# Kernel tuning notes

Hardware: AMD Instinct MI355X
Metric: run time of the kernel (lower is better)

Reference implementation:

```python
import jax, jax.numpy as jnp
import numpy as np

N = 50000      # nodes
E = 800000     # directed edges (avg degree 16)
F_IN = 128     # dataset.num_features
H = 256        # hidden_channels
C = 40         # dataset.num_classes


def _glorot(k, shape):
    lim = float(np.sqrt(6.0 / (shape[0] + shape[1])))
    return jax.random.uniform(k, shape, jnp.float32, -lim, lim)


def setup_inputs() -> dict:
    key = jax.random.key(0)
    ks = jax.random.split(key, 8)
    x = jax.random.normal(ks[0], (N, F_IN), jnp.float32)
    edge_index = jax.random.randint(ks[1], (2, E), 0, N, dtype=jnp.int32)
    W1 = _glorot(ks[2], (F_IN, H));      b1 = jnp.zeros((H,), jnp.float32)
    W2 = _glorot(ks[3], (H, H // 2));    b2 = jnp.zeros((H // 2,), jnp.float32)
    W3 = _glorot(ks[4], (H // 2, H // 4)); b3 = jnp.zeros((H // 4,), jnp.float32)
    W4 = _glorot(ks[5], (H // 4, C));    b4 = jnp.zeros((C,), jnp.float32)
    return {"x": x, "edge_index": edge_index,
            "W1": W1, "b1": b1, "W2": W2, "b2": b2,
            "W3": W3, "b3": b3, "W4": W4, "b4": b4}


def reference(x, edge_index, W1, b1, W2, b2, W3, b3, W4, b4):
    # GCNConv with default add_self_loops=True and symmetric normalization.
    loops = jnp.arange(N, dtype=edge_index.dtype)
    src = jnp.concatenate([edge_index[0], loops])   # message sources
    dst = jnp.concatenate([edge_index[1], loops])   # aggregation targets
    # degree computed on target index (PyG default), incl. self-loops
    deg = jax.ops.segment_sum(jnp.ones_like(dst, jnp.float32), dst, num_segments=N)
    dinv = jnp.where(deg > 0, jax.lax.rsqrt(deg), 0.0)
    norm = dinv[src] * dinv[dst]                    # [E+N]

    def conv(h, W, b):
        h = h @ W                                   # transform first (PyG order)
        msg = h[src] * norm[:, None]                # gather + scale
        return jax.ops.segment_sum(msg, dst, num_segments=N) + b

    h = jax.nn.relu(conv(x, W1, b1))   # dropout = identity in eval mode
    h = jax.nn.relu(conv(h, W2, b2))
    h = jax.nn.relu(conv(h, W3, b3))
    return conv(h, W4, b4)
```

## Files before the change

kernel.cpp:

```cpp
#include <hip/hip_runtime.h>
#include <stdint.h>

#define NNODES 50000
#define NEDGES 800000
#define NB ((NNODES + 255) / 256)
#define EPB 4096
#define SCAT_NBLK ((NEDGES + EPB - 1) / EPB)

typedef __attribute__((ext_vector_type(8))) short bf16x8;
typedef __attribute__((ext_vector_type(4))) float f32x4;

__device__ inline unsigned short f2bf(float f) {
    unsigned u = __float_as_uint(f);
    return (unsigned short)((u + 0x7fffu + ((u >> 16) & 1u)) >> 16);
}
__device__ inline float bf2f(unsigned short h) {
    return __uint_as_float(((unsigned)h) << 16);
}


__global__ void zero_kernel(int* __restrict__ p, int n) {
    int i = blockIdx.x * blockDim.x + threadIdx.x;
    if (i < n) p[i] = 0;
}

__global__ __launch_bounds__(256) void bucket_count_kernel(const int* __restrict__ dst,
                                                           int* __restrict__ bhist) {
    __shared__ int h[NB];
    for (int b = threadIdx.x; b < NB; b += 256) h[b] = 0;
    __syncthreads();
    const int base = blockIdx.x * EPB;
#pragma unroll
    for (int i = 0; i < EPB / 256; ++i) {
        const int e = base + threadIdx.x + i * 256;
        if (e < NEDGES) atomicAdd(&h[dst[e] >> 8], 1);
    }
    __syncthreads();
    for (int b = threadIdx.x; b < NB; b += 256)
        if (h[b]) atomicAdd(&bhist[b], h[b]);
}

__global__ __launch_bounds__(256) void bucket_scan_kernel(const int* __restrict__ bhist,
                                                          int* __restrict__ bofs,
                                                          int* __restrict__ gcur,
                                                          int* __restrict__ rp_last) {
    __shared__ int s[256];
    const int t = threadIdx.x;
    s[t] = (t < NB) ? bhist[t] : 0;
    __syncthreads();
    for (int off = 1; off < 256; off <<= 1) {
        int v = (t >= off) ? s[t - off] : 0;
        __syncthreads();
        s[t] += v;
        __syncthreads();
    }
    if (t < NB) {
        const int excl = (t > 0) ? s[t - 1] : 0;
        bofs[t] = excl;
        gcur[t] = excl;
    }
    if (t == 255) { bofs[NB] = s[255]; rp_last[0] = s[255]; }
}

__global__ __launch_bounds__(256) void bucket_scatter_kernel(const int* __restrict__ src,
                                                             const int* __restrict__ dst,
                                                             int* __restrict__ gcur,
                                                             unsigned* __restrict__ gpk) {
    __shared__ int h[256];
    __shared__ int s[256];
    __shared__ int gof[256];
    __shared__ unsigned pr[EPB];
    __shared__ int ga[EPB];

    const int t = threadIdx.x;
    const int base = blockIdx.x * EPB;
    const int nval = min(EPB, NEDGES - base);

    h[t] = 0;
    __syncthreads();
#pragma unroll
    for (int i = 0; i < EPB / 256; ++i) {
        const int e = base + t + i * 256;
        if (e < NEDGES) atomicAdd(&h[dst[e] >> 8], 1);
    }
    __syncthreads();
    s[t] = h[t];
    __syncthreads();
    for (int off = 1; off < 256; off <<= 1) {
        int v = (t >= off) ? s[t - off] : 0;
        __syncthreads();
        s[t] += v;
        __syncthreads();
    }
    {
        const int c = h[t];
        if (t < NB && c > 0) gof[t] = atomicAdd(&gcur[t], c);
        const int lofs = s[t] - c;
        h[t] = lofs;
        s[t] = lofs;
    }
    __syncthreads();
#pragma unroll
    for (int i = 0; i < EPB / 256; ++i) {
        const int e = base + t + i * 256;
        if (e < NEDGES) {
            const int d = dst[e];
            const int b = d >> 8;
            const int slot = atomicAdd(&h[b], 1);
            pr[slot] = ((unsigned)(d & 255) << 16) | (unsigned)src[e];
            ga[slot] = gof[b] + (slot - s[b]);
        }
    }
    __syncthreads();
#pragma unroll
    for (int i = 0; i < EPB / 256; ++i) {
        const int slot = t + i * 256;
        if (slot < nval) gpk[ga[slot]] = pr[slot];
    }
}

__global__ __launch_bounds__(256) void csr_fill_kernel(const unsigned* __restrict__ gpk,
                                                       const int* __restrict__ bofs,
                                                       int* __restrict__ rp,
                                                       float* __restrict__ dinv,
                                                       unsigned short* __restrict__ col) {
    __shared__ int c[256];
    __shared__ int s[256];
    __shared__ int cur[256];
    const int t = threadIdx.x;
    const int b = blockIdx.x;
    const int beg = bofs[b], end = bofs[b + 1];
    c[t] = 0;
    __syncthreads();
    for (int e = beg + t; e < end; e += 256) atomicAdd(&c[gpk[e] >> 16], 1);
    __syncthreads();
    s[t] = c[t];
    __syncthreads();
    for (int off = 1; off < 256; off <<= 1) {
        int v = (t >= off) ? s[t - off] : 0;
        __syncthreads();
        s[t] += v;
        __syncthreads();
    }
    const int excl = s[t] - c[t];
    cur[t] = excl;
    const int node = b * 256 + t;
    if (node < NNODES) {
        rp[node] = beg + excl;
        dinv[node] = rsqrtf((float)(c[t] + 1));
    }
    __syncthreads();
    for (int e = beg + t; e < end; e += 256) {
        const unsigned p = gpk[e];
        const int r = atomicAdd(&cur[p >> 16], 1);
        col[beg + r] = (unsigned short)(p & 0xffffu);
    }
}


__global__ __launch_bounds__(256) void cvt_kernel(const float* __restrict__ in,
                                                  const float* __restrict__ dinv,
                                                  unsigned short* __restrict__ out, int n4) {
    int i = blockIdx.x * 256 + threadIdx.x;
    if (i >= n4) return;
    const float dv = dinv[i >> 5];
    float4 v = *(const float4*)(in + (size_t)i * 4);
    ushort4 h;
    h.x = f2bf(dv * v.x); h.y = f2bf(dv * v.y); h.z = f2bf(dv * v.z); h.w = f2bf(dv * v.w);
    *(ushort4*)(out + (size_t)i * 4) = h;
}


template <bool RELU, bool HAS_BIAS>
__global__ __launch_bounds__(256) void agg128_kernel(const float* __restrict__ in32,
                                                     const unsigned short* __restrict__ inbf,
                                                     float* __restrict__ out,
                                                     const int* __restrict__ rp,
                                                     const unsigned short* __restrict__ col,
                                                     const float* __restrict__ dinv,
                                                     const float* __restrict__ bias) {
    const int wave = threadIdx.x >> 6;
    const int lane = threadIdx.x & 63;
    const int d = blockIdx.x * 4 + wave;
    if (d >= NNODES) return;
    const int quarter = lane >> 4;
    const int fl = lane & 15;
    const float dv = dinv[d];

    float acc[8] = {0.f, 0.f, 0.f, 0.f, 0.f, 0.f, 0.f, 0.f};
    if (quarter == 0) {
        float4 s0 = *(const float4*)(in32 + (size_t)d * 128 + fl * 8);
        float4 s1 = *(const float4*)(in32 + (size_t)d * 128 + fl * 8 + 4);
        acc[0] = dv * s0.x; acc[1] = dv * s0.y; acc[2] = dv * s0.z; acc[3] = dv * s0.w;
        acc[4] = dv * s1.x; acc[5] = dv * s1.y; acc[6] = dv * s1.z; acc[7] = dv * s1.w;
    }

    int j = rp[d] + quarter;
    const int end = rp[d + 1];
    for (; j + 12 < end; j += 16) {
        const int c0 = col[j], c1 = col[j + 4], c2 = col[j + 8], c3 = col[j + 12];
        bf16x8 a0 = *(const bf16x8*)(inbf + (size_t)c0 * 128 + fl * 8);
        bf16x8 a1 = *(const bf16x8*)(inbf + (size_t)c1 * 128 + fl * 8);
        bf16x8 a2 = *(const bf16x8*)(inbf + (size_t)c2 * 128 + fl * 8);
        bf16x8 a3 = *(const bf16x8*)(inbf + (size_t)c3 * 128 + fl * 8);
#pragma unroll
        for (int k = 0; k < 8; ++k)
            acc[k] += (bf2f((unsigned short)a0[k]) + bf2f((unsigned short)a1[k])) +
                      (bf2f((unsigned short)a2[k]) + bf2f((unsigned short)a3[k]));
    }
    for (; j + 4 < end; j += 8) {
        const int c0 = col[j], c1 = col[j + 4];
        bf16x8 a0 = *(const bf16x8*)(inbf + (size_t)c0 * 128 + fl * 8);
        bf16x8 a1 = *(const bf16x8*)(inbf + (size_t)c1 * 128 + fl * 8);
#pragma unroll
        for (int k = 0; k < 8; ++k)
            acc[k] += bf2f((unsigned short)a0[k]) + bf2f((unsigned short)a1[k]);
    }
    if (j < end) {
        const int c0 = col[j];
        bf16x8 a0 = *(const bf16x8*)(inbf + (size_t)c0 * 128 + fl * 8);
#pragma unroll
        for (int k = 0; k < 8; ++k) acc[k] += bf2f((unsigned short)a0[k]);
    }

#pragma unroll
    for (int v = 0; v < 8; ++v) {
        acc[v] += __shfl_down(acc[v], 32);
        acc[v] += __shfl_down(acc[v], 16);
    }

    if (quarter == 0) {
        float r[8];
#pragma unroll
        for (int v = 0; v < 8; ++v) {
            float t = dv * acc[v];
            if constexpr (HAS_BIAS) t += bias[fl * 8 + v];
            if constexpr (RELU) t = fmaxf(t, 0.0f);
            r[v] = t;
        }
        *(float4*)(out + (size_t)d * 128 + fl * 8)     = make_float4(r[0], r[1], r[2], r[3]);
        *(float4*)(out + (size_t)d * 128 + fl * 8 + 4) = make_float4(r[4], r[5], r[6], r[7]);
    }
}

template <bool RELU, bool HAS_BIAS, bool WRITE_BF>
__global__ __launch_bounds__(256) void agg64_kernel(const float* __restrict__ in32,
                                                    const unsigned short* __restrict__ inbf,
                                                    float* __restrict__ out,
                                                    unsigned short* __restrict__ outbf,
                                                    const int* __restrict__ rp,
                                                    const unsigned short* __restrict__ col,
                                                    const float* __restrict__ dinv,
                                                    const float* __restrict__ bias) {
    const int wave = threadIdx.x >> 6;
    const int lane = threadIdx.x & 63;
    const int d = blockIdx.x * 4 + wave;
    if (d >= NNODES) return;
    const int eighth = lane >> 3;
    const int fl = lane & 7;
    const float dv = dinv[d];

    float acc[8] = {0.f, 0.f, 0.f, 0.f, 0.f, 0.f, 0.f, 0.f};
    if (eighth == 0) {
        float4 s0 = *(const float4*)(in32 + (size_t)d * 64 + fl * 8);
        float4 s1 = *(const float4*)(in32 + (size_t)d * 64 + fl * 8 + 4);
        acc[0] = dv * s0.x; acc[1] = dv * s0.y; acc[2] = dv * s0.z; acc[3] = dv * s0.w;
        acc[4] = dv * s1.x; acc[5] = dv * s1.y; acc[6] = dv * s1.z; acc[7] = dv * s1.w;
    }

    int j = rp[d] + eighth;
    const int end = rp[d + 1];
    for (; j + 8 < end; j += 16) {
        const int c0 = col[j], c1 = col[j + 8];
        bf16x8 a0 = *(const bf16x8*)(inbf + (size_t)c0 * 64 + fl * 8);
        bf16x8 a1 = *(const bf16x8*)(inbf + (size_t)c1 * 64 + fl * 8);
#pragma unroll
        for (int k = 0; k < 8; ++k)
            acc[k] += bf2f((unsigned short)a0[k]) + bf2f((unsigned short)a1[k]);
    }
    if (j < end) {
        const int c0 = col[j];
        bf16x8 a0 = *(const bf16x8*)(inbf + (size_t)c0 * 64 + fl * 8);
#pragma unroll
        for (int k = 0; k < 8; ++k) acc[k] += bf2f((unsigned short)a0[k]);
    }

#pragma unroll
    for (int v = 0; v < 8; ++v) {
        acc[v] += __shfl_down(acc[v], 32);
        acc[v] += __shfl_down(acc[v], 16);
        acc[v] += __shfl_down(acc[v], 8);
    }

    if (eighth == 0) {
        float r[8];
#pragma unroll
        for (int v = 0; v < 8; ++v) {
            float t = dv * acc[v];
            if constexpr (HAS_BIAS) t += bias[fl * 8 + v];
            if constexpr (RELU) t = fmaxf(t, 0.0f);
            r[v] = t;
        }
        *(float4*)(out + (size_t)d * 64 + fl * 8)     = make_float4(r[0], r[1], r[2], r[3]);
        *(float4*)(out + (size_t)d * 64 + fl * 8 + 4) = make_float4(r[4], r[5], r[6], r[7]);
        if constexpr (WRITE_BF) {
            ushort4 h0, h1;
            h0.x = f2bf(dv * r[0]); h0.y = f2bf(dv * r[1]);
            h0.z = f2bf(dv * r[2]); h0.w = f2bf(dv * r[3]);
            h1.x = f2bf(dv * r[4]); h1.y = f2bf(dv * r[5]);
            h1.z = f2bf(dv * r[6]); h1.w = f2bf(dv * r[7]);
            *(ushort4*)(outbf + (size_t)d * 64 + fl * 8)     = h0;
            *(ushort4*)(outbf + (size_t)d * 64 + fl * 8 + 4) = h1;
        }
    }
}


template <int K, int M>
__global__ __launch_bounds__(256) void repack_kernel(const float* __restrict__ W,
                                                     unsigned short* __restrict__ hi,
                                                     unsigned short* __restrict__ lo) {
    int i = blockIdx.x * 256 + threadIdx.x;
    if (i >= K * M) return;
    const int k = i / M, n = i % M;
    constexpr int KS = K / 32;
    const int cb = n >> 7;
    const int ct = (n >> 4) & 7;
    const int ln = ((k >> 3) & 3) * 16 + (n & 15);
    const int j  = k & 7;
    const int ks = k >> 5;
    const size_t o = ((((size_t)cb * KS + ks) * 8 + ct) * 64 + ln) * 8 + j;
    const float f = W[i];
    const unsigned short h = f2bf(f);
    hi[o] = h;
    lo[o] = f2bf(f - bf2f(h));
}


template <int K, int M, int BM, bool BIAS_RELU, bool WRITE_BF>
__global__ __launch_bounds__(256) void mfma_gemm_kernel(const float* __restrict__ A,
                                                        const unsigned short* __restrict__ Whi,
                                                        const unsigned short* __restrict__ Wlo,
                                                        const float* __restrict__ bias,
                                                        float* __restrict__ C,
                                                        unsigned short* __restrict__ Cbf,
                                                        const float* __restrict__ dinv) {
    constexpr int KS = K / 32;
    constexpr int ASZ = BM * 64;
    constexpr int CI = (BM == 128) ? 4 : 2;
    __shared__ char lds[2 * ASZ + 16384];
    char* Ahi = lds;
    char* Alo = lds + ASZ;
    char* Bhi = lds + 2 * ASZ;
    char* Blo = lds + 2 * ASZ + 8192;

    const int t = threadIdx.x;
    const int lane = t & 63;
    const int w = t >> 6;
    const int wr = (BM == 128) ? (w >> 1) : 0;
    const int wc = (BM == 128) ? (w & 1) : w;
    const int r0 = blockIdx.x * BM;
    const int n0 = blockIdx.y * 128;

    const unsigned short* bhg = Whi + (size_t)blockIdx.y * KS * 4096;
    const unsigned short* blg = Wlo + (size_t)blockIdx.y * KS * 4096;

    f32x4 acc[4][CI];
#pragma unroll
    for (int i = 0; i < 4; ++i)
#pragma unroll
        for (int j = 0; j < CI; ++j) acc[i][j] = (f32x4){0.f, 0.f, 0.f, 0.f};

    for (int ks = 0; ks < KS; ++ks) {
        const int k0 = ks * 32;

        {
            const char* gh = (const char*)(bhg + (size_t)ks * 4096);
            const char* gl = (const char*)(blg + (size_t)ks * 4096);
#pragma unroll
            for (int c = 0; c < 2; ++c) {
                const int ct = w * 2 + c;
                __builtin_amdgcn_global_load_lds(
                    (const __attribute__((address_space(1))) void*)(gh + ct * 1024 + lane * 16),
                    (__attribute__((address_space(3))) void*)(Bhi + ct * 1024), 16, 0, 0);
                __builtin_amdgcn_global_load_lds(
                    (const __attribute__((address_space(1))) void*)(gl + ct * 1024 + lane * 16),
                    (__attribute__((address_space(3))) void*)(Blo + ct * 1024), 16, 0, 0);
            }
        }

        float4 av[BM / 32];
#pragma unroll
        for (int i = 0; i < BM / 32; ++i) {
            const int q = t + i * 256;
            const int row = q >> 3;
            const int kq = (q & 7) * 4;
            const int gr = r0 + row;
            float4 v = make_float4(0.f, 0.f, 0.f, 0.f);
            if (gr < NNODES) v = *(const float4*)(A + (size_t)gr * K + k0 + kq);
            av[i] = v;
        }
#pragma unroll
        for (int i = 0; i < BM / 32; ++i) {
            const int q = t + i * 256;
            const int row = q >> 3;
            const int kq = (q & 7) * 4;
            const int rt = row >> 4, m = row & 15, quad = kq >> 3, j0 = kq & 7;
            const int off = rt * 1024 + (quad * 16 + m) * 16 + j0 * 2;
            const float4 v = av[i];
            ushort4 h, l;
            h.x = f2bf(v.x); l.x = f2bf(v.x - bf2f(h.x));
            h.y = f2bf(v.y); l.y = f2bf(v.y - bf2f(h.y));
            h.z = f2bf(v.z); l.z = f2bf(v.z - bf2f(h.z));
            h.w = f2bf(v.w); l.w = f2bf(v.w - bf2f(h.w));
            *(ushort4*)(Ahi + off) = h;
            *(ushort4*)(Alo + off) = l;
        }
        __syncthreads();

        bf16x8 ah[4], al[4], bh[CI], bl[CI];
#pragma unroll
        for (int i = 0; i < 4; ++i) {
            ah[i] = *(const bf16x8*)(Ahi + (wr * 4 + i) * 1024 + lane * 16);
            al[i] = *(const bf16x8*)(Alo + (wr * 4 + i) * 1024 + lane * 16);
        }
#pragma unroll
        for (int j = 0; j < CI; ++j) {
            bh[j] = *(const bf16x8*)(Bhi + (wc * CI + j) * 1024 + lane * 16);
            bl[j] = *(const bf16x8*)(Blo + (wc * CI + j) * 1024 + lane * 16);
        }
#pragma unroll
        for (int i = 0; i < 4; ++i)
#pragma unroll
            for (int j = 0; j < CI; ++j) {
                acc[i][j] = __builtin_amdgcn_mfma_f32_16x16x32_bf16(ah[i], bh[j], acc[i][j], 0, 0, 0);
                acc[i][j] = __builtin_amdgcn_mfma_f32_16x16x32_bf16(ah[i], bl[j], acc[i][j], 0, 0, 0);
                acc[i][j] = __builtin_amdgcn_mfma_f32_16x16x32_bf16(al[i], bh[j], acc[i][j], 0, 0, 0);
            }
        __syncthreads();
    }

    const int quad = lane >> 4;
    const int cl = lane & 15;
#pragma unroll
    for (int i = 0; i < 4; ++i) {
#pragma unroll
        for (int j = 0; j < CI; ++j) {
            const int colg = n0 + wc * (CI * 16) + j * 16 + cl;
            float bv = 0.f;
            if constexpr (BIAS_RELU) bv = bias[colg];
#pragma unroll
            for (int r = 0; r < 4; ++r) {
                const int rowg = r0 + wr * 64 + i * 16 + quad * 4 + r;
                if (rowg < NNODES) {
                    float v = acc[i][j][r] + bv;
                    if constexpr (BIAS_RELU) v = fmaxf(v, 0.f);
                    C[(size_t)rowg * M + colg] = v;
                    if constexpr (WRITE_BF) Cbf[(size_t)rowg * M + colg] = f2bf(dinv[rowg] * v);
                }
            }
        }
    }
}


template <int BM, int BN, int BK, int TM, int TN, bool HAS_BIAS, bool RELU, bool WRITE_BF>
__global__ __launch_bounds__(256) void gemm_kernel(const float* __restrict__ A,
                                                   const float* __restrict__ W,
                                                   const float* __restrict__ bias,
                                                   float* __restrict__ C,
                                                   unsigned short* __restrict__ Cbf,
                                                   const float* __restrict__ dinv,
                                                   int Nrows, int K, int M) {
    constexpr int TX = BN / TN;
    constexpr int TY = BM / TM;
    static_assert(TX * TY == 256, "thread grid must be 256");
    constexpr int A_LOADS = (BM * BK) / (256 * 4);
    constexpr int W_LOADS = (BN * BK) / (256 * 4);
    static_assert(A_LOADS >= 1 && W_LOADS >= 1, "tile too small");

    const int tid = threadIdx.x;
    const int tx = tid % TX;
    const int ty = tid / TX;
    const int r0 = blockIdx.x * BM;
    const int c0 = blockIdx.y * BN;

    __shared__ float As[BK][BM + 4];
    __shared__ float Ws[BK][BN];

    float acc[TM][TN] = {};

    for (int k0 = 0; k0 < K; k0 += BK) {
#pragma unroll
        for (int l = 0; l < A_LOADS; ++l) {
            const int idx = tid + l * 256;
            const int row = idx / (BK / 4);
            const int kq = idx % (BK / 4);
            float4 v = make_float4(0.f, 0.f, 0.f, 0.f);
            const int gr = r0 + row;
            if (gr < Nrows) v = *(const float4*)(A + (size_t)gr * K + k0 + kq * 4);
            As[kq * 4 + 0][row] = v.x;
            As[kq * 4 + 1][row] = v.y;
            As[kq * 4 + 2][row] = v.z;
            As[kq * 4 + 3][row] = v.w;
        }
#pragma unroll
        for (int l = 0; l < W_LOADS; ++l) {
            const int idx = tid + l * 256;
            const int kk = idx / (BN / 4);
            const int cq = idx % (BN / 4);
            const int gc = c0 + cq * 4;
            float4 v;
            const float* wrow = W + (size_t)(k0 + kk) * M;
            if (gc + 3 < M) {
                v = *(const float4*)(wrow + gc);
            } else {
                v.x = (gc + 0 < M) ? wrow[gc + 0] : 0.f;
                v.y = (gc + 1 < M) ? wrow[gc + 1] : 0.f;
                v.z = (gc + 2 < M) ? wrow[gc + 2] : 0.f;
                v.w = (gc + 3 < M) ? wrow[gc + 3] : 0.f;
            }
            *(float4*)&Ws[kk][cq * 4] = v;
        }
        __syncthreads();

#pragma unroll
        for (int kk = 0; kk < BK; ++kk) {
            float a[TM], b[TN];
#pragma unroll
            for (int i = 0; i < TM; ++i) a[i] = As[kk][ty * TM + i];
#pragma unroll
            for (int j = 0; j < TN; ++j) b[j] = Ws[kk][tx * TN + j];
#pragma unroll
            for (int i = 0; i < TM; ++i)
#pragma unroll
                for (int j = 0; j < TN; ++j) acc[i][j] += a[i] * b[j];
        }
        __syncthreads();
    }

#pragma unroll
    for (int i = 0; i < TM; ++i) {
        const int gr = r0 + ty * TM + i;
        if (gr >= Nrows) continue;
        const float dvr = WRITE_BF ? dinv[gr] : 0.f;
#pragma unroll
        for (int j = 0; j < TN; ++j) {
            const int gc = c0 + tx * TN + j;
            if (gc >= M) continue;
            float v = acc[i][j];
            if constexpr (HAS_BIAS) v += bias[gc];
            if constexpr (RELU) v = fmaxf(v, 0.0f);
            C[(size_t)gr * M + gc] = v;
            if constexpr (WRITE_BF) Cbf[(size_t)gr * M + gc] = f2bf(dvr * v);
        }
    }
}


extern "C" void kernel_launch(void* const* d_in, const int* in_sizes, int n_in,
                              void* d_out, int out_size, void* d_ws, size_t ws_size,
                              hipStream_t stream) {
    const float* x  = (const float*)d_in[0];
    const int* ei   = (const int*)d_in[1];
    const float* W1 = (const float*)d_in[2];
    const float* b1 = (const float*)d_in[3];
    const float* W2 = (const float*)d_in[4];
    const float* b2 = (const float*)d_in[5];
    const float* W3 = (const float*)d_in[6];
    const float* b3 = (const float*)d_in[7];
    const float* W4 = (const float*)d_in[8];
    const float* b4 = (const float*)d_in[9];
    float* out = (float*)d_out;
    const int* esrc = ei;
    const int* edst = ei + NEDGES;

    char* w = (char*)d_ws;
    auto alloc = [&](size_t bytes) -> void* {
        void* p = (void*)w;
        w += (bytes + 255) & ~(size_t)255;
        return p;
    };
    int* rp     = (int*)alloc((size_t)(NNODES + 1) * 4);
    unsigned short* col = (unsigned short*)alloc((size_t)NEDGES * 2);
    float* dinv = (float*)alloc((size_t)NNODES * 4);
    int* bhist  = (int*)alloc((size_t)NB * 4);
    int* bofs   = (int*)alloc((size_t)(NB + 1) * 4);
    int* gcur   = (int*)alloc((size_t)NB * 4);
    unsigned* gpk = (unsigned*)alloc((size_t)NEDGES * 4);
    unsigned short* W1hi = (unsigned short*)alloc((size_t)128 * 256 * 2);
    unsigned short* W1lo = (unsigned short*)alloc((size_t)128 * 256 * 2);
    unsigned short* W2hi = (unsigned short*)alloc((size_t)256 * 128 * 2);
    unsigned short* W2lo = (unsigned short*)alloc((size_t)256 * 128 * 2);
    float* B0   = (float*)alloc((size_t)NNODES * 256 * 4);
    float* B1   = (float*)alloc((size_t)NNODES * 128 * 4);
    float* B2   = (float*)alloc((size_t)NNODES * 128 * 4);
    unsigned short* xbf  = (unsigned short*)alloc((size_t)NNODES * 128 * 2);
    unsigned short* B1bf = (unsigned short*)alloc((size_t)NNODES * 128 * 2);
    unsigned short* B0bf = (unsigned short*)alloc((size_t)NNODES * 64 * 2);
    unsigned short* B3bf = (unsigned short*)alloc((size_t)NNODES * 64 * 2);

    repack_kernel<128, 256><<<(128 * 256 + 255) / 256, 256, 0, stream>>>(W1, W1hi, W1lo);
    repack_kernel<256, 128><<<(256 * 128 + 255) / 256, 256, 0, stream>>>(W2, W2hi, W2lo);

    zero_kernel<<<1, 256, 0, stream>>>(bhist, NB);
    bucket_count_kernel<<<SCAT_NBLK, 256, 0, stream>>>(edst, bhist);
    bucket_scan_kernel<<<1, 256, 0, stream>>>(bhist, bofs, gcur, rp + NNODES);
    bucket_scatter_kernel<<<SCAT_NBLK, 256, 0, stream>>>(esrc, edst, gcur, gpk);
    csr_fill_kernel<<<NB, 256, 0, stream>>>(gpk, bofs, rp, dinv, col);

    cvt_kernel<<<(NNODES * 128 / 4 + 255) / 256, 256, 0, stream>>>(x, dinv, xbf, NNODES * 128 / 4);

    const int aggGrid = (NNODES + 3) / 4;
    const int rowBlks64 = (NNODES + 63) / 64;

    agg128_kernel<false, false><<<aggGrid, 256, 0, stream>>>(x, xbf, B2, rp, col, dinv, nullptr);
    mfma_gemm_kernel<128, 256, 64, true, false>
        <<<dim3(rowBlks64, 2), 256, 0, stream>>>(B2, W1hi, W1lo, b1, B0, nullptr, nullptr);

    mfma_gemm_kernel<256, 128, 64, false, true>
        <<<dim3(rowBlks64, 1), 256, 0, stream>>>(B0, W2hi, W2lo, nullptr, B1, B1bf, dinv);
    agg128_kernel<true, true><<<aggGrid, 256, 0, stream>>>(B1, B1bf, B2, rp, col, dinv, b2);

    gemm_kernel<64, 64, 16, 4, 4, false, false, true>
        <<<dim3(rowBlks64, 1), 256, 0, stream>>>(B2, W3, nullptr, B0, B0bf, dinv, NNODES, 128, 64);
    agg64_kernel<true, true, true><<<aggGrid, 256, 0, stream>>>(B0, B0bf, B1, B3bf, rp, col, dinv, b3);

    agg64_kernel<false, false, false><<<aggGrid, 256, 0, stream>>>(B1, B3bf, B2, nullptr, rp, col, dinv, nullptr);
    gemm_kernel<64, 64, 16, 4, 4, true, false, false>
        <<<dim3(rowBlks64, 1), 256, 0, stream>>>(B2, W4, b4, out, nullptr, nullptr, NNODES, 64, 40);
}
```

Baseline: 336.4 us.

## Fuse CSR build, weight repack and input convert into one cooperative kernel

Replaces eight small preprocessing launches (weight repack, histogram zero/count/scan/scatter, CSR fill, input convert) with a single cooperative kernel that uses grid-wide syncs between phases. It relies on NB (196) equalling the number of 4096-edge chunks, so one block covers both an edge chunk and a node bucket. Each block redoes the bucket scan locally instead of reading bofs. The goal is to remove launch gaps and tail effects, at the cost of grid.sync barriers and a redundant second histogram pass.

After: 514.1 us. 52.8% more time.

```diff
diff --git a/kernel.cpp b/kernel.cpp
--- a/kernel.cpp
+++ b/kernel.cpp
@@ -1,11 +1,13 @@
 #include <hip/hip_runtime.h>
+#include <hip/hip_cooperative_groups.h>
 #include <stdint.h>
+
+namespace cg = cooperative_groups;
 
 #define NNODES 50000
 #define NEDGES 800000
 #define NB ((NNODES + 255) / 256)
 #define EPB 4096
-#define SCAT_NBLK ((NEDGES + EPB - 1) / EPB)
 
 typedef __attribute__((ext_vector_type(8))) short bf16x8;
 typedef __attribute__((ext_vector_type(4))) float f32x4;
@@ -18,73 +20,71 @@
     return __uint_as_float(((unsigned)h) << 16);
 }
 
-
-__global__ void zero_kernel(int* __restrict__ p, int n) {
-    int i = blockIdx.x * blockDim.x + threadIdx.x;
-    if (i < n) p[i] = 0;
-}
-
-__global__ __launch_bounds__(256) void bucket_count_kernel(const int* __restrict__ dst,
-                                                           int* __restrict__ bhist) {
-    __shared__ int h[NB];
-    for (int b = threadIdx.x; b < NB; b += 256) h[b] = 0;
-    __syncthreads();
-    const int base = blockIdx.x * EPB;
-#pragma unroll
-    for (int i = 0; i < EPB / 256; ++i) {
-        const int e = base + threadIdx.x + i * 256;
-        if (e < NEDGES) atomicAdd(&h[dst[e] >> 8], 1);
-    }
-    __syncthreads();
-    for (int b = threadIdx.x; b < NB; b += 256)
-        if (h[b]) atomicAdd(&bhist[b], h[b]);
-}
-
-__global__ __launch_bounds__(256) void bucket_scan_kernel(const int* __restrict__ bhist,
-                                                          int* __restrict__ bofs,
-                                                          int* __restrict__ gcur,
-                                                          int* __restrict__ rp_last) {
-    __shared__ int s[256];
-    const int t = threadIdx.x;
-    s[t] = (t < NB) ? bhist[t] : 0;
-    __syncthreads();
-    for (int off = 1; off < 256; off <<= 1) {
-        int v = (t >= off) ? s[t - off] : 0;
-        __syncthreads();
-        s[t] += v;
-        __syncthreads();
-    }
-    if (t < NB) {
-        const int excl = (t > 0) ? s[t - 1] : 0;
-        bofs[t] = excl;
-        gcur[t] = excl;
-    }
-    if (t == 255) { bofs[NB] = s[255]; rp_last[0] = s[255]; }
-}
-
-__global__ __launch_bounds__(256) void bucket_scatter_kernel(const int* __restrict__ src,
-                                                             const int* __restrict__ dst,
-                                                             int* __restrict__ gcur,
-                                                             unsigned* __restrict__ gpk) {
+__device__ inline void repack_elem(const float* __restrict__ W, unsigned short* __restrict__ hi,
+                                   unsigned short* __restrict__ lo, int K, int M, int i) {
+    const int k = i / M, n = i % M;
+    const int KS = K / 32;
+    const int cb = n >> 7;
+    const int ct = (n >> 4) & 7;
+    const int ln = ((k >> 3) & 3) * 16 + (n & 15);
+    const int j  = k & 7;
+    const int ks = k >> 5;
+    const size_t o = ((((size_t)cb * KS + ks) * 8 + ct) * 64 + ln) * 8 + j;
+    const float f = W[i];
+    const unsigned short h = f2bf(f);
+    hi[o] = h;
+    lo[o] = f2bf(f - bf2f(h));
+}
+
+__global__ __launch_bounds__(256) void build_kernel(const int* __restrict__ src,
+                                                    const int* __restrict__ dst,
+                                                    const float* __restrict__ W1,
+                                                    const float* __restrict__ W2,
+                                                    unsigned short* __restrict__ W1hi,
+                                                    unsigned short* __restrict__ W1lo,
+                                                    unsigned short* __restrict__ W2hi,
+                                                    unsigned short* __restrict__ W2lo,
+                                                    int* __restrict__ bhist,
+                                                    int* __restrict__ gcur,
+                                                    unsigned* __restrict__ gpk,
+                                                    int* __restrict__ rp,
+                                                    float* __restrict__ dinv,
+                                                    unsigned short* __restrict__ col,
+                                                    const float* __restrict__ x,
+                                                    unsigned short* __restrict__ xbf) {
     __shared__ int h[256];
     __shared__ int s[256];
-    __shared__ int gof[256];
+    __shared__ int aux[256];
+    __shared__ float sdv[256];
     __shared__ unsigned pr[EPB];
     __shared__ int ga[EPB];
 
+    cg::grid_group grid = cg::this_grid();
     const int t = threadIdx.x;
-    const int base = blockIdx.x * EPB;
-    const int nval = min(EPB, NEDGES - base);
+    const int b = blockIdx.x;
+    const int NT = gridDim.x * 256;
+    const int gtid = b * 256 + t;
+
+    for (int i = gtid; i < 128 * 256; i += NT) repack_elem(W1, W1hi, W1lo, 128, 256, i);
+    for (int i = gtid; i < 256 * 128; i += NT) repack_elem(W2, W2hi, W2lo, 256, 128, i);
+    if (b == 0 && t < NB) bhist[t] = 0;
+    __threadfence();
+    grid.sync();
 
     h[t] = 0;
     __syncthreads();
+    const int base = b * EPB;
 #pragma unroll
     for (int i = 0; i < EPB / 256; ++i) {
         const int e = base + t + i * 256;
         if (e < NEDGES) atomicAdd(&h[dst[e] >> 8], 1);
     }
     __syncthreads();
-    s[t] = h[t];
+    if (t < NB && h[t]) atomicAdd(&bhist[t], h[t]);
+    __threadfence();
+    grid.sync();
+
+    s[t] = (t < NB) ? bhist[t] : 0;
     __syncthreads();
     for (int off = 1; off < 256; off <<= 1) {
         int v = (t >= off) ? s[t - off] : 0;
@@ -92,9 +92,35 @@
         s[t] += v;
         __syncthreads();
     }
+    const int my_beg = (b > 0) ? s[b - 1] : 0;
+    const int my_end = s[b];
+    if (b == 0) {
+        if (t < NB) gcur[t] = (t > 0) ? s[t - 1] : 0;
+        if (t == 255) rp[NNODES] = s[255];
+    }
+    __threadfence();
+    grid.sync();
+
+    const int nval = min(EPB, NEDGES - base);
+    h[t] = 0;
+    __syncthreads();
+#pragma unroll
+    for (int i = 0; i < EPB / 256; ++i) {
+        const int e = base + t + i * 256;
+        if (e < NEDGES) atomicAdd(&h[dst[e] >> 8], 1);
+    }
+    __syncthreads();
+    s[t] = h[t];
+    __syncthreads();
+    for (int off = 1; off < 256; off <<= 1) {
+        int v = (t >= off) ? s[t - off] : 0;
+        __syncthreads();
+        s[t] += v;
+        __syncthreads();
+    }
     {
         const int c = h[t];
-        if (t < NB && c > 0) gof[t] = atomicAdd(&gcur[t], c);
+        if (t < NB && c > 0) aux[t] = atomicAdd(&gcur[t], c);
         const int lofs = s[t] - c;
         h[t] = lofs;
         s[t] = lofs;
@@ -105,10 +131,10 @@
         const int e = base + t + i * 256;
         if (e < NEDGES) {
             const int d = dst[e];
-            const int b = d >> 8;
-            const int slot = atomicAdd(&h[b], 1);
+            const int bb = d >> 8;
+            const int slot = atomicAdd(&h[bb], 1);
             pr[slot] = ((unsigned)(d & 255) << 16) | (unsigned)src[e];
-            ga[slot] = gof[b] + (slot - s[b]);
+            ga[slot] = aux[bb] + (slot - s[bb]);
         }
     }
     __syncthreads();
@@ -117,24 +143,14 @@
         const int slot = t + i * 256;
         if (slot < nval) gpk[ga[slot]] = pr[slot];
     }
-}
-
-__global__ __launch_bounds__(256) void csr_fill_kernel(const unsigned* __restrict__ gpk,
-                                                       const int* __restrict__ bofs,
-                                                       int* __restrict__ rp,
-                                                       float* __restrict__ dinv,
-                                                       unsigned short* __restrict__ col) {
-    __shared__ int c[256];
-    __shared__ int s[256];
-    __shared__ int cur[256];
-    const int t = threadIdx.x;
-    const int b = blockIdx.x;
-    const int beg = bofs[b], end = bofs[b + 1];
-    c[t] = 0;
-    __syncthreads();
-    for (int e = beg + t; e < end; e += 256) atomicAdd(&c[gpk[e] >> 16], 1);
-    __syncthreads();
-    s[t] = c[t];
+    __threadfence();
+    grid.sync();
+
+    h[t] = 0;
+    __syncthreads();
+    for (int e = my_beg + t; e < my_end; e += 256) atomicAdd(&h[gpk[e] >> 16], 1);
+    __syncthreads();
+    s[t] = h[t];
     __syncthreads();
     for (int off = 1; off < 256; off <<= 1) {
         int v = (t >= off) ? s[t - off] : 0;
@@ -142,32 +158,33 @@
         s[t] += v;
         __syncthreads();
     }
-    const int excl = s[t] - c[t];
-    cur[t] = excl;
+    const int excl = s[t] - h[t];
+    aux[t] = excl;
     const int node = b * 256 + t;
+    const float dv = rsqrtf((float)(h[t] + 1));
+    sdv[t] = dv;
     if (node < NNODES) {
-        rp[node] = beg + excl;
-        dinv[node] = rsqrtf((float)(c[t] + 1));
-    }
-    __syncthreads();
-    for (int e = beg + t; e < end; e += 256) {
+        rp[node] = my_beg + excl;
+        dinv[node] = dv;
+    }
+    __syncthreads();
+    for (int e = my_beg + t; e < my_end; e += 256) {
         const unsigned p = gpk[e];
-        const int r = atomicAdd(&cur[p >> 16], 1);
-        col[beg + r] = (unsigned short)(p & 0xffffu);
-    }
-}
-
-
-__global__ __launch_bounds__(256) void cvt_kernel(const float* __restrict__ in,
-                                                  const float* __restrict__ dinv,
-                                                  unsigned short* __restrict__ out, int n4) {
-    int i = blockIdx.x * 256 + threadIdx.x;
-    if (i >= n4) return;
-    const float dv = dinv[i >> 5];
-    float4 v = *(const float4*)(in + (size_t)i * 4);
-    ushort4 h;
-    h.x = f2bf(dv * v.x); h.y = f2bf(dv * v.y); h.z = f2bf(dv * v.z); h.w = f2bf(dv * v.w);
-    *(ushort4*)(out + (size_t)i * 4) = h;
+        const int r = atomicAdd(&aux[p >> 16], 1);
+        col[my_beg + r] = (unsigned short)(p & 0xffffu);
+    }
+    const int nrows = min(256, NNODES - b * 256);
+    const float* xb = x + (size_t)b * 256 * 128;
+    unsigned short* ob = xbf + (size_t)b * 256 * 128;
+    const int n4 = nrows * 32;
+    for (int i = t; i < n4; i += 256) {
+        const float dv2 = sdv[i >> 5];
+        float4 v = *(const float4*)(xb + (size_t)i * 4);
+        ushort4 hh;
+        hh.x = f2bf(dv2 * v.x); hh.y = f2bf(dv2 * v.y);
+        hh.z = f2bf(dv2 * v.z); hh.w = f2bf(dv2 * v.w);
+        *(ushort4*)(ob + (size_t)i * 4) = hh;
+    }
 }
 
 
@@ -316,27 +333,6 @@
 }
 
 
-template <int K, int M>
-__global__ __launch_bounds__(256) void repack_kernel(const float* __restrict__ W,
-                                                     unsigned short* __restrict__ hi,
-                                                     unsigned short* __restrict__ lo) {
-    int i = blockIdx.x * 256 + threadIdx.x;
-    if (i >= K * M) return;
-    const int k = i / M, n = i % M;
-    constexpr int KS = K / 32;
-    const int cb = n >> 7;
-    const int ct = (n >> 4) & 7;
-    const int ln = ((k >> 3) & 3) * 16 + (n & 15);
-    const int j  = k & 7;
-    const int ks = k >> 5;
-    const size_t o = ((((size_t)cb * KS + ks) * 8 + ct) * 64 + ln) * 8 + j;
-    const float f = W[i];
-    const unsigned short h = f2bf(f);
-    hi[o] = h;
-    lo[o] = f2bf(f - bf2f(h));
-}
-
-
 template <int K, int M, int BM, bool BIAS_RELU, bool WRITE_BF>
 __global__ __launch_bounds__(256) void mfma_gemm_kernel(const float* __restrict__ A,
                                                         const unsigned short* __restrict__ Whi,
@@ -585,7 +581,6 @@
     unsigned short* col = (unsigned short*)alloc((size_t)NEDGES * 2);
     float* dinv = (float*)alloc((size_t)NNODES * 4);
     int* bhist  = (int*)alloc((size_t)NB * 4);
-    int* bofs   = (int*)alloc((size_t)(NB + 1) * 4);
     int* gcur   = (int*)alloc((size_t)NB * 4);
     unsigned* gpk = (unsigned*)alloc((size_t)NEDGES * 4);
     unsigned short* W1hi = (unsigned short*)alloc((size_t)128 * 256 * 2);
@@ -600,16 +595,13 @@
     unsigned short* B0bf = (unsigned short*)alloc((size_t)NNODES * 64 * 2);
     unsigned short* B3bf = (unsigned short*)alloc((size_t)NNODES * 64 * 2);
 
-    repack_kernel<128, 256><<<(128 * 256 + 255) / 256, 256, 0, stream>>>(W1, W1hi, W1lo);
-    repack_kernel<256, 128><<<(256 * 128 + 255) / 256, 256, 0, stream>>>(W2, W2hi, W2lo);
-
-    zero_kernel<<<1, 256, 0, stream>>>(bhist, NB);
-    bucket_count_kernel<<<SCAT_NBLK, 256, 0, stream>>>(edst, bhist);
-    bucket_scan_kernel<<<1, 256, 0, stream>>>(bhist, bofs, gcur, rp + NNODES);
-    bucket_scatter_kernel<<<SCAT_NBLK, 256, 0, stream>>>(esrc, edst, gcur, gpk);
-    csr_fill_kernel<<<NB, 256, 0, stream>>>(gpk, bofs, rp, dinv, col);
-
-    cvt_kernel<<<(NNODES * 128 / 4 + 255) / 256, 256, 0, stream>>>(x, dinv, xbf, NNODES * 128 / 4);
+    {
+        void* args[] = {(void*)&esrc, (void*)&edst, (void*)&W1, (void*)&W2,
+                        (void*)&W1hi, (void*)&W1lo, (void*)&W2hi, (void*)&W2lo,
+                        (void*)&bhist, (void*)&gcur, (void*)&gpk,
+                        (void*)&rp, (void*)&dinv, (void*)&col, (void*)&x, (void*)&xbf};
+        hipLaunchCooperativeKernel((void*)build_kernel, dim3(NB), dim3(256), args, 0, stream);
+    }
 
     const int aggGrid = (NNODES + 3) / 4;
     const int rowBlks64 = (NNODES + 63) / 64;
```

## Fuse preprocessing kernels and widen MFMA GEMM tile to full output width

Applied to the files above, without the earlier changes.

Merges the two weight-repack kernels and the histogram zeroing into one prep kernel, and folds the x-to-bf16 conversion into csr_fill so it uses dinv from shared memory. This cuts kernel launches and drops a separate dinv read. The MFMA GEMM loses the column-block grid dimension: each 64-row block now computes all M output columns, so the first GEMM reads its A tile only once. The cost is more accumulators per wave and more LDS per block, which may lower occupancy.

Result: slower. 345.6 us (+2.7%).

```diff
diff --git a/kernel.cpp b/kernel.cpp
--- a/kernel.cpp
+++ b/kernel.cpp
@@ -19,10 +19,35 @@
 }
 
 
-__global__ void zero_kernel(int* __restrict__ p, int n) {
-    int i = blockIdx.x * blockDim.x + threadIdx.x;
-    if (i < n) p[i] = 0;
-}
+__device__ inline void repack_elem(const float* __restrict__ W, unsigned short* __restrict__ hi,
+                                   unsigned short* __restrict__ lo, int K, int M, int i) {
+    const int k = i / M, n = i % M;
+    const int KS = K / 32;
+    const int cb = n >> 7;
+    const int ct = (n >> 4) & 7;
+    const int ln = ((k >> 3) & 3) * 16 + (n & 15);
+    const int j  = k & 7;
+    const int ks = k >> 5;
+    const size_t o = ((((size_t)cb * KS + ks) * 8 + ct) * 64 + ln) * 8 + j;
+    const float f = W[i];
+    const unsigned short h = f2bf(f);
+    hi[o] = h;
+    lo[o] = f2bf(f - bf2f(h));
+}
+
+__global__ __launch_bounds__(256) void prep_kernel(const float* __restrict__ W1,
+                                                   const float* __restrict__ W2,
+                                                   unsigned short* __restrict__ W1hi,
+                                                   unsigned short* __restrict__ W1lo,
+                                                   unsigned short* __restrict__ W2hi,
+                                                   unsigned short* __restrict__ W2lo,
+                                                   int* __restrict__ bhist) {
+    const int i = blockIdx.x * 256 + threadIdx.x;
+    if (i < 128 * 256) repack_elem(W1, W1hi, W1lo, 128, 256, i);
+    else repack_elem(W2, W2hi, W2lo, 256, 128, i - 128 * 256);
+    if (i < NB) bhist[i] = 0;
+}
+
 
 __global__ __launch_bounds__(256) void bucket_count_kernel(const int* __restrict__ dst,
                                                            int* __restrict__ bhist) {
@@ -123,10 +148,13 @@
                                                        const int* __restrict__ bofs,
                                                        int* __restrict__ rp,
                                                        float* __restrict__ dinv,
-                                                       unsigned short* __restrict__ col) {
+                                                       unsigned short* __restrict__ col,
+                                                       const float* __restrict__ x,
+                                                       unsigned short* __restrict__ xbf) {
     __shared__ int c[256];
     __shared__ int s[256];
     __shared__ int cur[256];
+    __shared__ float sdv[256];
     const int t = threadIdx.x;
     const int b = blockIdx.x;
     const int beg = bofs[b], end = bofs[b + 1];
@@ -145,9 +173,11 @@
     const int excl = s[t] - c[t];
     cur[t] = excl;
     const int node = b * 256 + t;
+    const float dv = rsqrtf((float)(c[t] + 1));
+    sdv[t] = dv;
     if (node < NNODES) {
         rp[node] = beg + excl;
-        dinv[node] = rsqrtf((float)(c[t] + 1));
+        dinv[node] = dv;
     }
     __syncthreads();
     for (int e = beg + t; e < end; e += 256) {
@@ -155,19 +185,18 @@
         const int r = atomicAdd(&cur[p >> 16], 1);
         col[beg + r] = (unsigned short)(p & 0xffffu);
     }
-}
-
-
-__global__ __launch_bounds__(256) void cvt_kernel(const float* __restrict__ in,
-                                                  const float* __restrict__ dinv,
-                                                  unsigned short* __restrict__ out, int n4) {
-    int i = blockIdx.x * 256 + threadIdx.x;
-    if (i >= n4) return;
-    const float dv = dinv[i >> 5];
-    float4 v = *(const float4*)(in + (size_t)i * 4);
-    ushort4 h;
-    h.x = f2bf(dv * v.x); h.y = f2bf(dv * v.y); h.z = f2bf(dv * v.z); h.w = f2bf(dv * v.w);
-    *(ushort4*)(out + (size_t)i * 4) = h;
+    const int nrows = min(256, NNODES - b * 256);
+    const float* xb = x + (size_t)b * 256 * 128;
+    unsigned short* ob = xbf + (size_t)b * 256 * 128;
+    const int n4 = nrows * 32;
+    for (int i = t; i < n4; i += 256) {
+        const float dv2 = sdv[i >> 5];
+        float4 v = *(const float4*)(xb + (size_t)i * 4);
+        ushort4 hh;
+        hh.x = f2bf(dv2 * v.x); hh.y = f2bf(dv2 * v.y);
+        hh.z = f2bf(dv2 * v.z); hh.w = f2bf(dv2 * v.w);
+        *(ushort4*)(ob + (size_t)i * 4) = hh;
+    }
 }
 
 
@@ -316,28 +345,7 @@
 }
 
 
-template <int K, int M>
-__global__ __launch_bounds__(256) void repack_kernel(const float* __restrict__ W,
-                                                     unsigned short* __restrict__ hi,
-                                                     unsigned short* __restrict__ lo) {
-    int i = blockIdx.x * 256 + threadIdx.x;
-    if (i >= K * M) return;
-    const int k = i / M, n = i % M;
-    constexpr int KS = K / 32;
-    const int cb = n >> 7;
-    const int ct = (n >> 4) & 7;
-    const int ln = ((k >> 3) & 3) * 16 + (n & 15);
-    const int j  = k & 7;
-    const int ks = k >> 5;
-    const size_t o = ((((size_t)cb * KS + ks) * 8 + ct) * 64 + ln) * 8 + j;
-    const float f = W[i];
-    const unsigned short h = f2bf(f);
-    hi[o] = h;
-    lo[o] = f2bf(f - bf2f(h));
-}
-
-
-template <int K, int M, int BM, bool BIAS_RELU, bool WRITE_BF>
+template <int K, int M, bool BIAS_RELU, bool WRITE_BF>
 __global__ __launch_bounds__(256) void mfma_gemm_kernel(const float* __restrict__ A,
                                                         const unsigned short* __restrict__ Whi,
                                                         const unsigned short* __restrict__ Wlo,
@@ -346,24 +354,17 @@
                                                         unsigned short* __restrict__ Cbf,
                                                         const float* __restrict__ dinv) {
     constexpr int KS = K / 32;
-    constexpr int ASZ = BM * 64;
-    constexpr int CI = (BM == 128) ? 4 : 2;
-    __shared__ char lds[2 * ASZ + 16384];
+    constexpr int CI = M / 64;
+    __shared__ char lds[8192 + 2 * M * 64];
     char* Ahi = lds;
-    char* Alo = lds + ASZ;
-    char* Bhi = lds + 2 * ASZ;
-    char* Blo = lds + 2 * ASZ + 8192;
+    char* Alo = lds + 4096;
+    char* Bhi = lds + 8192;
+    char* Blo = lds + 8192 + M * 64;
 
     const int t = threadIdx.x;
     const int lane = t & 63;
     const int w = t >> 6;
-    const int wr = (BM == 128) ? (w >> 1) : 0;
-    const int wc = (BM == 128) ? (w & 1) : w;
-    const int r0 = blockIdx.x * BM;
-    const int n0 = blockIdx.y * 128;
-
-    const unsigned short* bhg = Whi + (size_t)blockIdx.y * KS * 4096;
-    const unsigned short* blg = Wlo + (size_t)blockIdx.y * KS * 4096;
+    const int r0 = blockIdx.x * 64;
 
     f32x4 acc[4][CI];
 #pragma unroll
@@ -375,23 +376,22 @@
         const int k0 = ks * 32;
 
         {
-            const char* gh = (const char*)(bhg + (size_t)ks * 4096);
-            const char* gl = (const char*)(blg + (size_t)ks * 4096);
-#pragma unroll
-            for (int c = 0; c < 2; ++c) {
-                const int ct = w * 2 + c;
+#pragma unroll
+            for (int c = 0; c < CI; ++c) {
+                const int g = w * CI + c;
+                const size_t srcb = ((size_t)((g >> 3) * KS + ks) * 8 + (g & 7)) * 1024;
                 __builtin_amdgcn_global_load_lds(
-                    (const __attribute__((address_space(1))) void*)(gh + ct * 1024 + lane * 16),
-                    (__attribute__((address_space(3))) void*)(Bhi + ct * 1024), 16, 0, 0);
+                    (const __attribute__((address_space(1))) void*)((const char*)Whi + srcb + lane * 16),
+                    (__attribute__((address_space(3))) void*)(Bhi + g * 1024), 16, 0, 0);
                 __builtin_amdgcn_global_load_lds(
-                    (const __attribute__((address_space(1))) void*)(gl + ct * 1024 + lane * 16),
-                    (__attribute__((address_space(3))) void*)(Blo + ct * 1024), 16, 0, 0);
+                    (const __attribute__((address_space(1))) void*)((const char*)Wlo + srcb + lane * 16),
+                    (__attribute__((address_space(3))) void*)(Blo + g * 1024), 16, 0, 0);
             }
         }
 
-        float4 av[BM / 32];
-#pragma unroll
-        for (int i = 0; i < BM / 32; ++i) {
+        float4 av[2];
+#pragma unroll
+        for (int i = 0; i < 2; ++i) {
             const int q = t + i * 256;
             const int row = q >> 3;
             const int kq = (q & 7) * 4;
@@ -401,7 +401,7 @@
             av[i] = v;
         }
 #pragma unroll
-        for (int i = 0; i < BM / 32; ++i) {
+        for (int i = 0; i < 2; ++i) {
             const int q = t + i * 256;
             const int row = q >> 3;
             const int kq = (q & 7) * 4;
@@ -421,13 +421,13 @@
         bf16x8 ah[4], al[4], bh[CI], bl[CI];
 #pragma unroll
         for (int i = 0; i < 4; ++i) {
-            ah[i] = *(const bf16x8*)(Ahi + (wr * 4 + i) * 1024 + lane * 16);
-            al[i] = *(const bf16x8*)(Alo + (wr * 4 + i) * 1024 + lane * 16);
+            ah[i] = *(const bf16x8*)(Ahi + i * 1024 + lane * 16);
+            al[i] = *(const bf16x8*)(Alo + i * 1024 + lane * 16);
         }
 #pragma unroll
         for (int j = 0; j < CI; ++j) {
-            bh[j] = *(const bf16x8*)(Bhi + (wc * CI + j) * 1024 + lane * 16);
-            bl[j] = *(const bf16x8*)(Blo + (wc * CI + j) * 1024 + lane * 16);
+            bh[j] = *(const bf16x8*)(Bhi + (w * CI + j) * 1024 + lane * 16);
+            bl[j] = *(const bf16x8*)(Blo + (w * CI + j) * 1024 + lane * 16);
         }
 #pragma unroll
         for (int i = 0; i < 4; ++i)
@@ -446,12 +446,12 @@
     for (int i = 0; i < 4; ++i) {
 #pragma unroll
         for (int j = 0; j < CI; ++j) {
-            const int colg = n0 + wc * (CI * 16) + j * 16 + cl;
+            const int colg = (w * CI + j) * 16 + cl;
             float bv = 0.f;
             if constexpr (BIAS_RELU) bv = bias[colg];
 #pragma unroll
             for (int r = 0; r < 4; ++r) {
-                const int rowg = r0 + wr * 64 + i * 16 + quad * 4 + r;
+                const int rowg = r0 + i * 16 + quad * 4 + r;
                 if (rowg < NNODES) {
                     float v = acc[i][j][r] + bv;
                     if constexpr (BIAS_RELU) v = fmaxf(v, 0.f);
@@ -600,26 +600,23 @@
     unsigned short* B0bf = (unsigned short*)alloc((size_t)NNODES * 64 * 2);
     unsigned short* B3bf = (unsigned short*)alloc((size_t)NNODES * 64 * 2);
 
-    repack_kernel<128, 256><<<(128 * 256 + 255) / 256, 256, 0, stream>>>(W1, W1hi, W1lo);
-    repack_kernel<256, 128><<<(256 * 128 + 255) / 256, 256, 0, stream>>>(W2, W2hi, W2lo);
-
-    zero_kernel<<<1, 256, 0, stream>>>(bhist, NB);
+    prep_kernel<<<(128 * 256 + 256 * 128) / 256, 256, 0, stream>>>(
+        W1, W2, W1hi, W1lo, W2hi, W2lo, bhist);
+
     bucket_count_kernel<<<SCAT_NBLK, 256, 0, stream>>>(edst, bhist);
     bucket_scan_kernel<<<1, 256, 0, stream>>>(bhist, bofs, gcur, rp + NNODES);
     bucket_scatter_kernel<<<SCAT_NBLK, 256, 0, stream>>>(esrc, edst, gcur, gpk);
-    csr_fill_kernel<<<NB, 256, 0, stream>>>(gpk, bofs, rp, dinv, col);
-
-    cvt_kernel<<<(NNODES * 128 / 4 + 255) / 256, 256, 0, stream>>>(x, dinv, xbf, NNODES * 128 / 4);
+    csr_fill_kernel<<<NB, 256, 0, stream>>>(gpk, bofs, rp, dinv, col, x, xbf);
 
     const int aggGrid = (NNODES + 3) / 4;
     const int rowBlks64 = (NNODES + 63) / 64;
 
     agg128_kernel<false, false><<<aggGrid, 256, 0, stream>>>(x, xbf, B2, rp, col, dinv, nullptr);
-    mfma_gemm_kernel<128, 256, 64, true, false>
-        <<<dim3(rowBlks64, 2), 256, 0, stream>>>(B2, W1hi, W1lo, b1, B0, nullptr, nullptr);
-
-    mfma_gemm_kernel<256, 128, 64, false, true>
-        <<<dim3(rowBlks64, 1), 256, 0, stream>>>(B0, W2hi, W2lo, nullptr, B1, B1bf, dinv);
+    mfma_gemm_kernel<128, 256, true, false>
+        <<<rowBlks64, 256, 0, stream>>>(B2, W1hi, W1lo, b1, B0, nullptr, nullptr);
+
+    mfma_gemm_kernel<256, 128, false, true>
+        <<<rowBlks64, 256, 0, stream>>>(B0, W2hi, W2lo, nullptr, B1, B1bf, dinv);
     agg128_kernel<true, true><<<aggGrid, 256, 0, stream>>>(B1, B1bf, B2, rp, col, dinv, b2);
 
     gemm_kernel<64, 64, 16, 4, 4, false, false, true>
```
